# Performance work log

Measured on AMD Instinct MI355X. Metric: run time of the kernel, lower is better.

Reference implementation:

```python
import jax, jax.numpy as jnp
import numpy as np

B, L, S, H, E, D = 4, 2048, 2048, 8, 64, 64

def setup_inputs() -> dict:
    key = jax.random.key(0)
    kq, kk, kv = jax.random.split(key, 3)
    queries = jax.random.normal(kq, (B, L, H, E), dtype=jnp.float32)
    keys = jax.random.normal(kk, (B, S, H, E), dtype=jnp.float32)
    values = jax.random.normal(kv, (B, S, H, D), dtype=jnp.float32)
    # TriangularCausalMask: True above the diagonal (positions to mask)
    causal = jnp.triu(jnp.ones((L, S), dtype=bool), k=1)
    attn_mask = jnp.broadcast_to(causal[None, None], (B, 1, L, S))
    return {"queries": queries, "keys": keys, "values": values, "attn_mask": attn_mask}

def reference(queries, keys, values, attn_mask):
    scale = 1.0 / jnp.sqrt(jnp.asarray(E, queries.dtype))
    # scores: [B,H,L,S]
    scores = jnp.einsum('blhe,bshe->bhls', queries, keys)
    neg_inf = jnp.asarray(-jnp.inf, scores.dtype)
    scores = jnp.where(attn_mask, neg_inf, scores)
    A = jax.nn.softmax(scale * scores, axis=-1)
    # dropout is identity in eval mode
    V = jnp.einsum('bhls,bshd->blhd', A, values)
    return V
```

## Files before the change

kernel.cpp:

```cpp
#include <hip/hip_runtime.h>
#include <math.h>

typedef __attribute__((ext_vector_type(8))) short bf16x8;
typedef __attribute__((ext_vector_type(4))) float f32x4;
typedef __attribute__((ext_vector_type(4))) unsigned int u32x4;

#define B_ 4
#define L_ 2048
#define S_ 2048
#define H_ 8
#define E_ 64
#define D_ 64
#define NT_ 32
#define TILE_BYTES 16384
#define WS_NEEDED ((size_t)B_ * H_ * NT_ * TILE_BYTES)
#define SCL (0.125f * 1.44269504088896f)

__device__ __forceinline__ unsigned short f2bf(float x) {
    unsigned int u = __builtin_bit_cast(unsigned int, x);
    u += 0x7fffu + ((u >> 16) & 1u);
    return (unsigned short)(u >> 16);
}
__device__ __forceinline__ int rho(int r) {
    return (r & 32) | (((r >> 2) & 1) << 4) | (((r >> 3) & 3) << 2) | (r & 3);
}

__global__ __launch_bounds__(256) void prep_kv(const float* __restrict__ K,
                                               const float* __restrict__ V,
                                               unsigned short* __restrict__ ws)
{
    __shared__ __align__(16) unsigned short vt[64][80];
    const int tid = threadIdx.x;
    const int bid = blockIdx.x;
    const int kt  = bid >> 5;
    const int bh  = (((bid >> 3) & 3) << 3) | (bid & 7);
    const int b   = bh >> 3, h = bh & 7;
    const int s0  = kt * 64;
    const int r   = tid >> 2;
    const int e0  = (tid & 3) * 16;

    const float* krow = K + (((size_t)(b * S_ + s0 + r)) * H_ + h) * E_ + e0;
    const float* vrow = V + (((size_t)(b * S_ + s0 + r)) * H_ + h) * D_ + e0;
    char* tile = (char*)(ws) + ((size_t)(bh * NT_ + kt) * TILE_BYTES);

    unsigned short kb[16];
    #pragma unroll
    for (int i = 0; i < 4; ++i) {
        f32x4 k4 = *(const f32x4*)(krow + i * 4);
        #pragma unroll
        for (int jq = 0; jq < 4; ++jq) kb[i * 4 + jq] = f2bf(k4[jq]);
    }
    {
        const int rr = rho(r);
        const int m  = (rr & 7) << 4;
        char* kbase = tile + rr * 128;
        u32x4 lo, hi;
        #pragma unroll
        for (int jq = 0; jq < 4; ++jq) {
            lo[jq] = (unsigned)kb[2 * jq] | ((unsigned)kb[2 * jq + 1] << 16);
            hi[jq] = (unsigned)kb[8 + 2 * jq] | ((unsigned)kb[9 + 2 * jq] << 16);
        }
        *(u32x4*)(kbase + ((2 * e0) ^ m))      = lo;
        *(u32x4*)(kbase + ((2 * e0 + 16) ^ m)) = hi;
    }
    #pragma unroll
    for (int i = 0; i < 4; ++i) {
        f32x4 v4 = *(const f32x4*)(vrow + i * 4);
        #pragma unroll
        for (int jq = 0; jq < 4; ++jq) vt[e0 + i * 4 + jq][r] = f2bf(v4[jq]);
    }
    __syncthreads();
    {
        const int d  = tid >> 2;
        const int c0 = (tid & 3) * 16;
        const int m  = (d & 7) << 4;
        char* vbase = tile + 8192 + d * 128;
        u32x4 lo = *(const u32x4*)&vt[d][c0];
        u32x4 hi = *(const u32x4*)&vt[d][c0 + 8];
        *(u32x4*)(vbase + ((2 * c0) ^ m))      = lo;
        *(u32x4*)(vbase + ((2 * c0 + 16) ^ m)) = hi;
    }
}

#define GL16(dst, p, o) asm volatile("global_load_dwordx4 %0, %1, off offset:" o \
                                     : "=&v"(dst) : "v"(p) : "memory")

#define ISSUE_K() do { \
    GL16(ka[0], pKa, "-3072"); GL16(ka[1], pKb, "-3072"); \
    GL16(ka[2], pKa, "-1024"); GL16(ka[3], pKb, "-1024"); \
    GL16(ka[4], pKa, "1024");  GL16(ka[5], pKb, "1024");  \
    GL16(ka[6], pKa, "3072");  GL16(ka[7], pKb, "3072"); } while (0)

#define ISSUE_V() do { \
    GL16(vb[0], pVa, "-3072"); GL16(vb[1], pVb, "-3072"); \
    GL16(vb[2], pVa, "-1024"); GL16(vb[3], pVb, "-1024"); \
    GL16(vb[4], pVa, "1024");  GL16(vb[5], pVb, "1024");  \
    GL16(vb[6], pVa, "3072");  GL16(vb[7], pVb, "3072"); } while (0)

__device__ __forceinline__ void do_tile(
    const float* __restrict__ Q, const char* __restrict__ tb,
    int b0, int h, int qt, int nt, int lq, int g, float* __restrict__ O)
{
    int qrow[2];
    qrow[0] = qt * 32 + lq;
    qrow[1] = qt * 32 + 16 + lq;

    bf16x8 qf[2][2];
    #pragma unroll
    for (int qs = 0; qs < 2; ++qs) {
        const float* qptr = Q + (((size_t)(b0 * L_ + qrow[qs])) * H_ + h) * E_;
        #pragma unroll
        for (int eb = 0; eb < 2; ++eb) {
            const float* pq = qptr + eb * 32 + g * 8;
            f32x4 a = *(const f32x4*)pq;
            f32x4 b = *(const f32x4*)(pq + 4);
            bf16x8 qv;
            #pragma unroll
            for (int k = 0; k < 4; ++k) {
                qv[k]     = (short)f2bf(a[k] * SCL);
                qv[4 + k] = (short)f2bf(b[k] * SCL);
            }
            qf[qs][eb] = qv;
        }
    }

    const int mm  = (lq & 7) << 4;
    const char* pKa = tb + lq * 128 + ((16 * g) ^ mm) + 3072;
    const char* pKb = tb + lq * 128 + ((64 + 16 * g) ^ mm) + 3072;
    const char* pVa = pKa + 8192;
    const char* pVb = pKb + 8192;

    u32x4 ka[8], vb[8];
    f32x4 acc[2][4] = {};
    float ls[2] = {0.f, 0.f};

    ISSUE_K();
    ISSUE_V();

    for (int kt = 0; kt < nt; ++kt) {
        asm volatile("s_waitcnt vmcnt(8)" ::: "memory");
        __builtin_amdgcn_sched_barrier(0);

        f32x4 sc[2][4];
        __builtin_amdgcn_s_setprio(1);
        #pragma unroll
        for (int st = 0; st < 4; ++st) {
            bf16x8 k0 = __builtin_bit_cast(bf16x8, ka[2 * st]);
            bf16x8 k1 = __builtin_bit_cast(bf16x8, ka[2 * st + 1]);
            #pragma unroll
            for (int qs = 0; qs < 2; ++qs) {
                f32x4 z = {0.f, 0.f, 0.f, 0.f};
                f32x4 cc = __builtin_amdgcn_mfma_f32_16x16x32_bf16(k0, qf[qs][0], z, 0, 0, 0);
                sc[qs][st] = __builtin_amdgcn_mfma_f32_16x16x32_bf16(k1, qf[qs][1], cc, 0, 0, 0);
            }
        }
        __builtin_amdgcn_s_setprio(0);

        const bool hasnext = (kt + 1 < nt);
        if (hasnext) { pKa += TILE_BYTES; pKb += TILE_BYTES; ISSUE_K(); }

        const int kv0 = kt * 64;
        u32x4 pw[2][2];
        #pragma unroll
        for (int qs = 0; qs < 2; ++qs) {
            #pragma unroll
            for (int st = 0; st < 4; ++st) {
                f32x4 cc = sc[qs][st];
                if (kt == nt - 1) {
                    #pragma unroll
                    for (int r = 0; r < 4; ++r) {
                        const int kv = kv0 + 32 * (st >> 1) + 8 * g + 4 * (st & 1) + r;
                        if (kv > qrow[qs]) cc[r] = -INFINITY;
                    }
                }
                f32x4 ev;
                #pragma unroll
                for (int r = 0; r < 4; ++r)
                    asm("v_exp_f32 %0, %1" : "=v"(ev[r]) : "v"(cc[r]));
                ls[qs] += (ev[0] + ev[1]) + (ev[2] + ev[3]);
                asm("v_cvt_pk_bf16_f32 %0, %1, %2" : "=v"(pw[qs][st >> 1][2 * (st & 1)])     : "v"(ev[0]), "v"(ev[1]));
                asm("v_cvt_pk_bf16_f32 %0, %1, %2" : "=v"(pw[qs][st >> 1][2 * (st & 1) + 1]) : "v"(ev[2]), "v"(ev[3]));
            }
        }

        if (hasnext) asm volatile("s_waitcnt vmcnt(8)" ::: "memory");
        else         asm volatile("s_waitcnt vmcnt(0)" ::: "memory");
        __builtin_amdgcn_sched_barrier(0);

        __builtin_amdgcn_s_setprio(1);
        #pragma unroll
        for (int dt = 0; dt < 4; ++dt) {
            bf16x8 v0 = __builtin_bit_cast(bf16x8, vb[2 * dt]);
            bf16x8 v1 = __builtin_bit_cast(bf16x8, vb[2 * dt + 1]);
            #pragma unroll
            for (int qs = 0; qs < 2; ++qs) {
                acc[qs][dt] = __builtin_amdgcn_mfma_f32_16x16x32_bf16(v0, __builtin_bit_cast(bf16x8, pw[qs][0]), acc[qs][dt], 0, 0, 0);
                acc[qs][dt] = __builtin_amdgcn_mfma_f32_16x16x32_bf16(v1, __builtin_bit_cast(bf16x8, pw[qs][1]), acc[qs][dt], 0, 0, 0);
            }
        }
        __builtin_amdgcn_s_setprio(0);

        if (hasnext) { pVa += TILE_BYTES; pVb += TILE_BYTES; ISSUE_V(); }
    }

    #pragma unroll
    for (int qs = 0; qs < 2; ++qs) {
        float l = ls[qs] + __shfl_xor(ls[qs], 16);
        l += __shfl_xor(l, 32);
        const float inv = 1.0f / l;
        float* op = O + (((size_t)(b0 * L_ + qrow[qs])) * H_ + h) * D_;
        #pragma unroll
        for (int dt = 0; dt < 4; ++dt) {
            f32x4 o;
            #pragma unroll
            for (int r = 0; r < 4; ++r) o[r] = acc[qs][dt][r] * inv;
            *(f32x4*)(op + dt * 16 + 4 * g) = o;
        }
    }
}

__global__ __launch_bounds__(128, 2) void attn8(const float* __restrict__ Q,
                                                const unsigned short* __restrict__ ws,
                                                float* __restrict__ O)
{
    const int tid  = threadIdx.x;
    const int lane = tid & 63;
    const int w    = tid >> 6;
    const int lq   = lane & 15;
    const int g    = lane >> 4;

    const int bid = blockIdx.x;
    const int bh  = bid & 31;
    const int jj  = bid >> 5;
    const int b0  = bh >> 3, h = bh & 7;

    const int p   = jj * 2 + w;
    const int ntA = (p >> 1) + 1;
    const int ntB = ((63 - p) >> 1) + 1;

    const char* tb = (const char*)ws + (size_t)bh * NT_ * TILE_BYTES;

    do_tile(Q, tb, b0, h, p,      ntA, lq, g, O);
    do_tile(Q, tb, b0, h, 63 - p, ntB, lq, g, O);
}

#define KPITCH 72
__global__ __launch_bounds__(256, 2) void attn_fwd_fb(
    const float* __restrict__ Q, const float* __restrict__ K,
    const float* __restrict__ V, float* __restrict__ O)
{
    __shared__ unsigned short Klds[64 * KPITCH];
    __shared__ unsigned short Vlds[64 * KPITCH];
    const int tid = threadIdx.x, lane = tid & 63, w = tid >> 6;
    const int lq = lane & 15, g = lane >> 4;
    const int bid = blockIdx.x, qb = bid & 31, bh = bid >> 5;
    const int b0 = bh >> 3, h = bh & 7;
    const int q0 = qb * 64, qrow = q0 + w * 16 + lq;
    const float* qptr = Q + ((size_t)(b0 * L_ + qrow) * H_ + h) * E_;
    bf16x8 qf[2];
    #pragma unroll
    for (int eb = 0; eb < 2; ++eb) {
        const float* pp = qptr + eb * 32 + g * 8;
        f32x4 a = *(const f32x4*)pp; f32x4 b = *(const f32x4*)(pp + 4);
        bf16x8 q;
        #pragma unroll
        for (int jq = 0; jq < 4; ++jq) { q[jq] = (short)f2bf(a[jq] * 0.125f); q[4 + jq] = (short)f2bf(b[jq] * 0.125f); }
        qf[eb] = q;
    }
    const int tr = tid >> 2, tc = tid & 3;
    const int rh = rho(tr);
    f32x4 acc[4] = {};
    float mrow = -INFINITY, lrow = 0.f;
    for (int kt = 0; kt < qb + 1; ++kt) {
        const int kv0 = kt * 64;
        __syncthreads();
        {
            const float* krow = K + ((size_t)((b0 * S_ + kv0 + tr)) * H_ + h) * E_;
            const float* vrow = V + ((size_t)((b0 * S_ + kv0 + tr)) * H_ + h) * D_;
            #pragma unroll
            for (int i = 0; i < 4; ++i) {
                const int e0 = tc * 4 + i * 16;
                f32x4 k4 = *(const f32x4*)(krow + e0);
                unsigned int lo = (unsigned)f2bf(k4[0]) | ((unsigned)f2bf(k4[1]) << 16);
                unsigned int hi = (unsigned)f2bf(k4[2]) | ((unsigned)f2bf(k4[3]) << 16);
                *(uint2*)&Klds[rh * KPITCH + e0] = make_uint2(lo, hi);
                f32x4 v4 = *(const f32x4*)(vrow + e0);
                #pragma unroll
                for (int k2 = 0; k2 < 4; ++k2) Vlds[(e0 + k2) * KPITCH + tr] = f2bf(v4[k2]);
            }
        }
        __syncthreads();
        f32x4 sc[4];
        #pragma unroll
        for (int st = 0; st < 4; ++st) {
            const unsigned short* kr = &Klds[(st * 16 + lq) * KPITCH];
            bf16x8 ka0 = *(const bf16x8*)(kr + 8 * g);
            bf16x8 ka1 = *(const bf16x8*)(kr + 32 + 8 * g);
            f32x4 cc = {0.f, 0.f, 0.f, 0.f};
            cc = __builtin_amdgcn_mfma_f32_16x16x32_bf16(ka0, qf[0], cc, 0, 0, 0);
            cc = __builtin_amdgcn_mfma_f32_16x16x32_bf16(ka1, qf[1], cc, 0, 0, 0);
            sc[st] = cc;
        }
        float tmax = -INFINITY;
        #pragma unroll
        for (int st = 0; st < 4; ++st) {
            const int kvb = kv0 + 32 * (st >> 1) + 8 * g + 4 * (st & 1);
            #pragma unroll
            for (int r = 0; r < 4; ++r) { if (kvb + r > qrow) sc[st][r] = -INFINITY; tmax = fmaxf(tmax, sc[st][r]); }
        }
        tmax = fmaxf(tmax, __shfl_xor(tmax, 16));
        tmax = fmaxf(tmax, __shfl_xor(tmax, 32));
        const float mnew = fmaxf(mrow, tmax);
        const float corr = __expf(mrow - mnew);
        float pv[4][4]; float tsum = 0.f;
        #pragma unroll
        for (int st = 0; st < 4; ++st)
            #pragma unroll
            for (int r = 0; r < 4; ++r) { float e = __expf(sc[st][r] - mnew); pv[st][r] = e; tsum += e; }
        tsum += __shfl_xor(tsum, 16); tsum += __shfl_xor(tsum, 32);
        lrow = lrow * corr + tsum; mrow = mnew;
        #pragma unroll
        for (int dt = 0; dt < 4; ++dt)
            #pragma unroll
            for (int r = 0; r < 4; ++r) acc[dt][r] *= corr;
        bf16x8 pb[2];
        #pragma unroll
        for (int bb = 0; bb < 2; ++bb)
            #pragma unroll
            for (int s = 0; s < 2; ++s)
                #pragma unroll
                for (int r = 0; r < 4; ++r) pb[bb][4 * s + r] = (short)f2bf(pv[2 * bb + s][r]);
        #pragma unroll
        for (int bb = 0; bb < 2; ++bb)
            #pragma unroll
            for (int dt = 0; dt < 4; ++dt) {
                bf16x8 va = *(const bf16x8*)&Vlds[(dt * 16 + lq) * KPITCH + 32 * bb + 8 * g];
                acc[dt] = __builtin_amdgcn_mfma_f32_16x16x32_bf16(va, pb[bb], acc[dt], 0, 0, 0);
            }
    }
    const float inv = 1.0f / lrow;
    float* optr = O + ((size_t)(b0 * L_ + qrow) * H_ + h) * D_;
    #pragma unroll
    for (int dt = 0; dt < 4; ++dt) {
        f32x4 o;
        #pragma unroll
        for (int r = 0; r < 4; ++r) o[r] = acc[dt][r] * inv;
        *(f32x4*)(optr + dt * 16 + 4 * g) = o;
    }
}

extern "C" void kernel_launch(void* const* d_in, const int* in_sizes, int n_in,
                              void* d_out, int out_size, void* d_ws, size_t ws_size,
                              hipStream_t stream) {
    const float* Q = (const float*)d_in[0];
    const float* K = (const float*)d_in[1];
    const float* V = (const float*)d_in[2];
    float* O = (float*)d_out;
    if (ws_size >= WS_NEEDED) {
        prep_kv<<<dim3(B_ * H_ * NT_), 256, 0, stream>>>(K, V, (unsigned short*)d_ws);
        attn8<<<dim3(512), 128, 0, stream>>>(Q, (const unsigned short*)d_ws, O);
    } else {
        attn_fwd_fb<<<dim3(B_ * H_ * 32), 256, 0, stream>>>(Q, K, V, O);
    }
}
```

Baseline: 49.08 us.

## Share K/V tiles across 8 waves via LDS double buffering with global_load_lds

```diff
diff --git a/kernel.cpp b/kernel.cpp
--- a/kernel.cpp
+++ b/kernel.cpp
@@ -23,6 +23,10 @@
 }
 __device__ __forceinline__ int rho(int r) {
     return (r & 32) | (((r >> 2) & 1) << 4) | (((r >> 3) & 3) << 2) | (r & 3);
+}
+__device__ __forceinline__ void gload16(const void* g, void* l) {
+    __builtin_amdgcn_global_load_lds((const __attribute__((address_space(1))) unsigned int*)g,
+                                     (__attribute__((address_space(3))) unsigned int*)l, 16, 0, 0);
 }
 
 __global__ __launch_bounds__(256) void prep_kv(const float* __restrict__ K,
@@ -82,28 +86,29 @@
     }
 }
 
-#define GL16(dst, p, o) asm volatile("global_load_dwordx4 %0, %1, off offset:" o \
-                                     : "=&v"(dst) : "v"(p) : "memory")
-
-#define ISSUE_K() do { \
-    GL16(ka[0], pKa, "-3072"); GL16(ka[1], pKb, "-3072"); \
-    GL16(ka[2], pKa, "-1024"); GL16(ka[3], pKb, "-1024"); \
-    GL16(ka[4], pKa, "1024");  GL16(ka[5], pKb, "1024");  \
-    GL16(ka[6], pKa, "3072");  GL16(ka[7], pKb, "3072"); } while (0)
-
-#define ISSUE_V() do { \
-    GL16(vb[0], pVa, "-3072"); GL16(vb[1], pVb, "-3072"); \
-    GL16(vb[2], pVa, "-1024"); GL16(vb[3], pVb, "-1024"); \
-    GL16(vb[4], pVa, "1024");  GL16(vb[5], pVb, "1024");  \
-    GL16(vb[6], pVa, "3072");  GL16(vb[7], pVb, "3072"); } while (0)
-
-__device__ __forceinline__ void do_tile(
-    const float* __restrict__ Q, const char* __restrict__ tb,
-    int b0, int h, int qt, int nt, int lq, int g, float* __restrict__ O)
+__global__ __launch_bounds__(512, 4) void attn9(const float* __restrict__ Q,
+                                                const unsigned short* __restrict__ ws,
+                                                float* __restrict__ O)
 {
+    __shared__ __align__(16) char lds[2][TILE_BYTES];
+
+    const int tid  = threadIdx.x;
+    const int lane = tid & 63;
+    const int w    = tid >> 6;
+    const int lq   = lane & 15;
+    const int g    = lane >> 4;
+
+    const int bid = blockIdx.x;
+    const int bh  = bid & 31;
+    const int j   = bid >> 5;
+    const int b0  = bh >> 3, h = bh & 7;
+
+    const int q0  = j * 256 + w * 32;
+    const int nt  = 4 * j + 4;
+    const int dkt = 4 * j + (w >> 1);
     int qrow[2];
-    qrow[0] = qt * 32 + lq;
-    qrow[1] = qt * 32 + 16 + lq;
+    qrow[0] = q0 + lq;
+    qrow[1] = q0 + 16 + lq;
 
     bf16x8 qf[2][2];
     #pragma unroll
@@ -124,83 +129,83 @@
         }
     }
 
-    const int mm  = (lq & 7) << 4;
-    const char* pKa = tb + lq * 128 + ((16 * g) ^ mm) + 3072;
-    const char* pKb = tb + lq * 128 + ((64 + 16 * g) ^ mm) + 3072;
-    const char* pVa = pKa + 8192;
-    const char* pVb = pKb + 8192;
-
-    u32x4 ka[8], vb[8];
     f32x4 acc[2][4] = {};
     float ls[2] = {0.f, 0.f};
 
-    ISSUE_K();
-    ISSUE_V();
-
+    const char* tb = (const char*)ws + (size_t)bh * NT_ * TILE_BYTES;
+
+    gload16(tb + tid * 16, &lds[0][tid * 16]);
+    gload16(tb + 8192 + tid * 16, &lds[0][8192 + tid * 16]);
+
+    int cur = 0;
     for (int kt = 0; kt < nt; ++kt) {
-        asm volatile("s_waitcnt vmcnt(8)" ::: "memory");
+        if (kt + 1 < nt) {
+            const char* gp = tb + (size_t)(kt + 1) * TILE_BYTES;
+            char* lp = &lds[cur ^ 1][0];
+            gload16(gp + tid * 16, lp + tid * 16);
+            gload16(gp + 8192 + tid * 16, lp + 8192 + tid * 16);
+            asm volatile("s_waitcnt vmcnt(2)" ::: "memory");
+        } else {
+            asm volatile("s_waitcnt vmcnt(0)" ::: "memory");
+        }
+        __builtin_amdgcn_s_barrier();
         __builtin_amdgcn_sched_barrier(0);
 
-        f32x4 sc[2][4];
-        __builtin_amdgcn_s_setprio(1);
-        #pragma unroll
-        for (int st = 0; st < 4; ++st) {
-            bf16x8 k0 = __builtin_bit_cast(bf16x8, ka[2 * st]);
-            bf16x8 k1 = __builtin_bit_cast(bf16x8, ka[2 * st + 1]);
-            #pragma unroll
-            for (int qs = 0; qs < 2; ++qs) {
-                f32x4 z = {0.f, 0.f, 0.f, 0.f};
-                f32x4 cc = __builtin_amdgcn_mfma_f32_16x16x32_bf16(k0, qf[qs][0], z, 0, 0, 0);
-                sc[qs][st] = __builtin_amdgcn_mfma_f32_16x16x32_bf16(k1, qf[qs][1], cc, 0, 0, 0);
-            }
-        }
-        __builtin_amdgcn_s_setprio(0);
-
-        const bool hasnext = (kt + 1 < nt);
-        if (hasnext) { pKa += TILE_BYTES; pKb += TILE_BYTES; ISSUE_K(); }
-
-        const int kv0 = kt * 64;
-        u32x4 pw[2][2];
-        #pragma unroll
-        for (int qs = 0; qs < 2; ++qs) {
+        if (kt <= dkt) {
+            const char* Kl = &lds[cur][0];
+            const char* Vl = &lds[cur][8192];
+            const int kv0 = kt * 64;
+
+            u32x4 pw[2][2];
             #pragma unroll
             for (int st = 0; st < 4; ++st) {
-                f32x4 cc = sc[qs][st];
-                if (kt == nt - 1) {
+                const int row = st * 16 + lq;
+                const int mm = (row & 7) << 4;
+                const char* kr = Kl + row * 128;
+                bf16x8 k0 = *(const bf16x8*)(kr + ((16 * g) ^ mm));
+                bf16x8 k1 = *(const bf16x8*)(kr + ((64 + 16 * g) ^ mm));
+                #pragma unroll
+                for (int qs = 0; qs < 2; ++qs) {
+                    f32x4 z = {0.f, 0.f, 0.f, 0.f};
+                    __builtin_amdgcn_s_setprio(1);
+                    f32x4 cc = __builtin_amdgcn_mfma_f32_16x16x32_bf16(k0, qf[qs][0], z, 0, 0, 0);
+                    cc = __builtin_amdgcn_mfma_f32_16x16x32_bf16(k1, qf[qs][1], cc, 0, 0, 0);
+                    __builtin_amdgcn_s_setprio(0);
+                    if (kt == dkt) {
+                        #pragma unroll
+                        for (int r = 0; r < 4; ++r) {
+                            const int kv = kv0 + 32 * (st >> 1) + 8 * g + 4 * (st & 1) + r;
+                            if (kv > qrow[qs]) cc[r] = -INFINITY;
+                        }
+                    }
+                    f32x4 ev;
                     #pragma unroll
-                    for (int r = 0; r < 4; ++r) {
-                        const int kv = kv0 + 32 * (st >> 1) + 8 * g + 4 * (st & 1) + r;
-                        if (kv > qrow[qs]) cc[r] = -INFINITY;
-                    }
+                    for (int r = 0; r < 4; ++r)
+                        asm("v_exp_f32 %0, %1" : "=v"(ev[r]) : "v"(cc[r]));
+                    ls[qs] += (ev[0] + ev[1]) + (ev[2] + ev[3]);
+                    asm("v_cvt_pk_bf16_f32 %0, %1, %2" : "=v"(pw[qs][st >> 1][2 * (st & 1)])     : "v"(ev[0]), "v"(ev[1]));
+                    asm("v_cvt_pk_bf16_f32 %0, %1, %2" : "=v"(pw[qs][st >> 1][2 * (st & 1) + 1]) : "v"(ev[2]), "v"(ev[3]));
                 }
-                f32x4 ev;
+            }
+
+            #pragma unroll
+            for (int dt = 0; dt < 4; ++dt) {
+                const int row = dt * 16 + lq;
+                const int mm = (row & 7) << 4;
+                bf16x8 v0 = *(const bf16x8*)(Vl + row * 128 + ((16 * g) ^ mm));
+                bf16x8 v1 = *(const bf16x8*)(Vl + row * 128 + ((64 + 16 * g) ^ mm));
+                __builtin_amdgcn_s_setprio(1);
                 #pragma unroll
-                for (int r = 0; r < 4; ++r)
-                    asm("v_exp_f32 %0, %1" : "=v"(ev[r]) : "v"(cc[r]));
-                ls[qs] += (ev[0] + ev[1]) + (ev[2] + ev[3]);
-                asm("v_cvt_pk_bf16_f32 %0, %1, %2" : "=v"(pw[qs][st >> 1][2 * (st & 1)])     : "v"(ev[0]), "v"(ev[1]));
-                asm("v_cvt_pk_bf16_f32 %0, %1, %2" : "=v"(pw[qs][st >> 1][2 * (st & 1) + 1]) : "v"(ev[2]), "v"(ev[3]));
-            }
-        }
-
-        if (hasnext) asm volatile("s_waitcnt vmcnt(8)" ::: "memory");
-        else         asm volatile("s_waitcnt vmcnt(0)" ::: "memory");
-        __builtin_amdgcn_sched_barrier(0);
-
-        __builtin_amdgcn_s_setprio(1);
-        #pragma unroll
-        for (int dt = 0; dt < 4; ++dt) {
-            bf16x8 v0 = __builtin_bit_cast(bf16x8, vb[2 * dt]);
-            bf16x8 v1 = __builtin_bit_cast(bf16x8, vb[2 * dt + 1]);
-            #pragma unroll
-            for (int qs = 0; qs < 2; ++qs) {
-                acc[qs][dt] = __builtin_amdgcn_mfma_f32_16x16x32_bf16(v0, __builtin_bit_cast(bf16x8, pw[qs][0]), acc[qs][dt], 0, 0, 0);
-                acc[qs][dt] = __builtin_amdgcn_mfma_f32_16x16x32_bf16(v1, __builtin_bit_cast(bf16x8, pw[qs][1]), acc[qs][dt], 0, 0, 0);
-            }
-        }
-        __builtin_amdgcn_s_setprio(0);
-
-        if (hasnext) { pVa += TILE_BYTES; pVb += TILE_BYTES; ISSUE_V(); }
+                for (int qs = 0; qs < 2; ++qs) {
+                    acc[qs][dt] = __builtin_amdgcn_mfma_f32_16x16x32_bf16(v0, __builtin_bit_cast(bf16x8, pw[qs][0]), acc[qs][dt], 0, 0, 0);
+                    acc[qs][dt] = __builtin_amdgcn_mfma_f32_16x16x32_bf16(v1, __builtin_bit_cast(bf16x8, pw[qs][1]), acc[qs][dt], 0, 0, 0);
+                }
+                __builtin_amdgcn_s_setprio(0);
+            }
+        }
+
+        __builtin_amdgcn_s_barrier();
+        cur ^= 1;
     }
 
     #pragma unroll
@@ -217,31 +222,6 @@
             *(f32x4*)(op + dt * 16 + 4 * g) = o;
         }
     }
-}
-
-__global__ __launch_bounds__(128, 2) void attn8(const float* __restrict__ Q,
-                                                const unsigned short* __restrict__ ws,
-                                                float* __restrict__ O)
-{
-    const int tid  = threadIdx.x;
-    const int lane = tid & 63;
-    const int w    = tid >> 6;
-    const int lq   = lane & 15;
-    const int g    = lane >> 4;
-
-    const int bid = blockIdx.x;
-    const int bh  = bid & 31;
-    const int jj  = bid >> 5;
-    const int b0  = bh >> 3, h = bh & 7;
-
-    const int p   = jj * 2 + w;
-    const int ntA = (p >> 1) + 1;
-    const int ntB = ((63 - p) >> 1) + 1;
-
-    const char* tb = (const char*)ws + (size_t)bh * NT_ * TILE_BYTES;
-
-    do_tile(Q, tb, b0, h, p,      ntA, lq, g, O);
-    do_tile(Q, tb, b0, h, 63 - p, ntB, lq, g, O);
 }
 
 #define KPITCH 72
@@ -358,7 +338,7 @@
     float* O = (float*)d_out;
     if (ws_size >= WS_NEEDED) {
         prep_kv<<<dim3(B_ * H_ * NT_), 256, 0, stream>>>(K, V, (unsigned short*)d_ws);
-        attn8<<<dim3(512), 128, 0, stream>>>(Q, (const unsigned short*)d_ws, O);
+        attn9<<<dim3(256), 512, 0, stream>>>(Q, (const unsigned short*)d_ws, O);
     } else {
         attn_fwd_fb<<<dim3(B_ * H_ * 32), 256, 0, stream>>>(Q, K, V, O);
     }
```

Result: slower. 56.20 us (+14.5%).

## Double-buffer K/V register prefetch two tiles ahead and use 4-wave blocks

Applied to the files above, without the earlier changes.

```diff
diff --git a/kernel.cpp b/kernel.cpp
--- a/kernel.cpp
+++ b/kernel.cpp
@@ -85,22 +85,89 @@
 #define GL16(dst, p, o) asm volatile("global_load_dwordx4 %0, %1, off offset:" o \
                                      : "=&v"(dst) : "v"(p) : "memory")
 
-#define ISSUE_K() do { \
-    GL16(ka[0], pKa, "-3072"); GL16(ka[1], pKb, "-3072"); \
-    GL16(ka[2], pKa, "-1024"); GL16(ka[3], pKb, "-1024"); \
-    GL16(ka[4], pKa, "1024");  GL16(ka[5], pKb, "1024");  \
-    GL16(ka[6], pKa, "3072");  GL16(ka[7], pKb, "3072"); } while (0)
-
-#define ISSUE_V() do { \
-    GL16(vb[0], pVa, "-3072"); GL16(vb[1], pVb, "-3072"); \
-    GL16(vb[2], pVa, "-1024"); GL16(vb[3], pVb, "-1024"); \
-    GL16(vb[4], pVa, "1024");  GL16(vb[5], pVb, "1024");  \
-    GL16(vb[6], pVa, "3072");  GL16(vb[7], pVb, "3072"); } while (0)
-
-__device__ __forceinline__ void do_tile(
+#define ISSUE8(ARR, BA, BB) do { \
+    GL16(ARR[0], BA, "-3072"); GL16(ARR[1], BB, "-3072"); \
+    GL16(ARR[2], BA, "-1024"); GL16(ARR[3], BB, "-1024"); \
+    GL16(ARR[4], BA, "1024");  GL16(ARR[5], BB, "1024");  \
+    GL16(ARR[6], BA, "3072");  GL16(ARR[7], BB, "3072"); } while (0)
+
+#define TRIP_HALF(KARR, VARR, KT) do { \
+    asm volatile("s_waitcnt vmcnt(24)" ::: "memory"); \
+    __builtin_amdgcn_sched_barrier(0); \
+    const bool act_ = (KT) < nt; \
+    f32x4 sc[2][4]; \
+    if (act_) { \
+        __builtin_amdgcn_s_setprio(1); \
+        _Pragma("unroll") \
+        for (int st = 0; st < 4; ++st) { \
+            bf16x8 k0 = __builtin_bit_cast(bf16x8, KARR[2 * st]); \
+            bf16x8 k1 = __builtin_bit_cast(bf16x8, KARR[2 * st + 1]); \
+            _Pragma("unroll") \
+            for (int qs = 0; qs < 2; ++qs) { \
+                f32x4 z = {0.f, 0.f, 0.f, 0.f}; \
+                f32x4 cc = __builtin_amdgcn_mfma_f32_16x16x32_bf16(k0, qf[qs][0], z, 0, 0, 0); \
+                sc[qs][st] = __builtin_amdgcn_mfma_f32_16x16x32_bf16(k1, qf[qs][1], cc, 0, 0, 0); \
+            } \
+        } \
+        __builtin_amdgcn_s_setprio(0); \
+    } \
+    { int ti = (KT) + 2; if (ti > nm1) ti = nm1; \
+      const char* ba_ = tb + (size_t)ti * TILE_BYTES + o_a; \
+      const char* bb_ = tb + (size_t)ti * TILE_BYTES + o_b; \
+      ISSUE8(KARR, ba_, bb_); } \
+    u32x4 pw[2][2]; \
+    if (act_) { \
+        const int kv0 = (KT) * 64; \
+        const bool maskit = ((KT) == nm1); \
+        _Pragma("unroll") \
+        for (int qs = 0; qs < 2; ++qs) { \
+            _Pragma("unroll") \
+            for (int st = 0; st < 4; ++st) { \
+                f32x4 cc = sc[qs][st]; \
+                if (maskit) { \
+                    _Pragma("unroll") \
+                    for (int r = 0; r < 4; ++r) { \
+                        const int kv = kv0 + 32 * (st >> 1) + 8 * g + 4 * (st & 1) + r; \
+                        if (kv > qrow[qs]) cc[r] = -INFINITY; \
+                    } \
+                } \
+                f32x4 ev; \
+                _Pragma("unroll") \
+                for (int r = 0; r < 4; ++r) \
+                    asm("v_exp_f32 %0, %1" : "=v"(ev[r]) : "v"(cc[r])); \
+                ls[qs] += (ev[0] + ev[1]) + (ev[2] + ev[3]); \
+                asm("v_cvt_pk_bf16_f32 %0, %1, %2" : "=v"(pw[qs][st >> 1][2 * (st & 1)])     : "v"(ev[0]), "v"(ev[1])); \
+                asm("v_cvt_pk_bf16_f32 %0, %1, %2" : "=v"(pw[qs][st >> 1][2 * (st & 1) + 1]) : "v"(ev[2]), "v"(ev[3])); \
+            } \
+        } \
+    } \
+    asm volatile("s_waitcnt vmcnt(24)" ::: "memory"); \
+    __builtin_amdgcn_sched_barrier(0); \
+    if (act_) { \
+        __builtin_amdgcn_s_setprio(1); \
+        _Pragma("unroll") \
+        for (int dt = 0; dt < 4; ++dt) { \
+            bf16x8 v0 = __builtin_bit_cast(bf16x8, VARR[2 * dt]); \
+            bf16x8 v1 = __builtin_bit_cast(bf16x8, VARR[2 * dt + 1]); \
+            _Pragma("unroll") \
+            for (int qs = 0; qs < 2; ++qs) { \
+                acc[qs][dt] = __builtin_amdgcn_mfma_f32_16x16x32_bf16(v0, __builtin_bit_cast(bf16x8, pw[qs][0]), acc[qs][dt], 0, 0, 0); \
+                acc[qs][dt] = __builtin_amdgcn_mfma_f32_16x16x32_bf16(v1, __builtin_bit_cast(bf16x8, pw[qs][1]), acc[qs][dt], 0, 0, 0); \
+            } \
+        } \
+        __builtin_amdgcn_s_setprio(0); \
+    } \
+    { int ti = (KT) + 2; if (ti > nm1) ti = nm1; \
+      const char* ba_ = tb + (size_t)ti * TILE_BYTES + 8192 + o_a; \
+      const char* bb_ = tb + (size_t)ti * TILE_BYTES + 8192 + o_b; \
+      ISSUE8(VARR, ba_, bb_); } \
+} while (0)
+
+__device__ __forceinline__ void do_tile16(
     const float* __restrict__ Q, const char* __restrict__ tb,
     int b0, int h, int qt, int nt, int lq, int g, float* __restrict__ O)
 {
+    const int nm1 = nt - 1;
     int qrow[2];
     qrow[0] = qt * 32 + lq;
     qrow[1] = qt * 32 + 16 + lq;
@@ -125,83 +192,31 @@
     }
 
     const int mm  = (lq & 7) << 4;
-    const char* pKa = tb + lq * 128 + ((16 * g) ^ mm) + 3072;
-    const char* pKb = tb + lq * 128 + ((64 + 16 * g) ^ mm) + 3072;
-    const char* pVa = pKa + 8192;
-    const char* pVb = pKb + 8192;
-
-    u32x4 ka[8], vb[8];
+    const int o_a = lq * 128 + ((16 * g) ^ mm) + 3072;
+    const int o_b = lq * 128 + ((64 + 16 * g) ^ mm) + 3072;
+
+    u32x4 kA[8], kB[8], vA[8], vB[8];
     f32x4 acc[2][4] = {};
     float ls[2] = {0.f, 0.f};
 
-    ISSUE_K();
-    ISSUE_V();
-
-    for (int kt = 0; kt < nt; ++kt) {
-        asm volatile("s_waitcnt vmcnt(8)" ::: "memory");
-        __builtin_amdgcn_sched_barrier(0);
-
-        f32x4 sc[2][4];
-        __builtin_amdgcn_s_setprio(1);
-        #pragma unroll
-        for (int st = 0; st < 4; ++st) {
-            bf16x8 k0 = __builtin_bit_cast(bf16x8, ka[2 * st]);
-            bf16x8 k1 = __builtin_bit_cast(bf16x8, ka[2 * st + 1]);
-            #pragma unroll
-            for (int qs = 0; qs < 2; ++qs) {
-                f32x4 z = {0.f, 0.f, 0.f, 0.f};
-                f32x4 cc = __builtin_amdgcn_mfma_f32_16x16x32_bf16(k0, qf[qs][0], z, 0, 0, 0);
-                sc[qs][st] = __builtin_amdgcn_mfma_f32_16x16x32_bf16(k1, qf[qs][1], cc, 0, 0, 0);
-            }
-        }
-        __builtin_amdgcn_s_setprio(0);
-
-        const bool hasnext = (kt + 1 < nt);
-        if (hasnext) { pKa += TILE_BYTES; pKb += TILE_BYTES; ISSUE_K(); }
-
-        const int kv0 = kt * 64;
-        u32x4 pw[2][2];
-        #pragma unroll
-        for (int qs = 0; qs < 2; ++qs) {
-            #pragma unroll
-            for (int st = 0; st < 4; ++st) {
-                f32x4 cc = sc[qs][st];
-                if (kt == nt - 1) {
-                    #pragma unroll
-                    for (int r = 0; r < 4; ++r) {
-                        const int kv = kv0 + 32 * (st >> 1) + 8 * g + 4 * (st & 1) + r;
-                        if (kv > qrow[qs]) cc[r] = -INFINITY;
-                    }
-                }
-                f32x4 ev;
-                #pragma unroll
-                for (int r = 0; r < 4; ++r)
-                    asm("v_exp_f32 %0, %1" : "=v"(ev[r]) : "v"(cc[r]));
-                ls[qs] += (ev[0] + ev[1]) + (ev[2] + ev[3]);
-                asm("v_cvt_pk_bf16_f32 %0, %1, %2" : "=v"(pw[qs][st >> 1][2 * (st & 1)])     : "v"(ev[0]), "v"(ev[1]));
-                asm("v_cvt_pk_bf16_f32 %0, %1, %2" : "=v"(pw[qs][st >> 1][2 * (st & 1) + 1]) : "v"(ev[2]), "v"(ev[3]));
-            }
-        }
-
-        if (hasnext) asm volatile("s_waitcnt vmcnt(8)" ::: "memory");
-        else         asm volatile("s_waitcnt vmcnt(0)" ::: "memory");
-        __builtin_amdgcn_sched_barrier(0);
-
-        __builtin_amdgcn_s_setprio(1);
-        #pragma unroll
-        for (int dt = 0; dt < 4; ++dt) {
-            bf16x8 v0 = __builtin_bit_cast(bf16x8, vb[2 * dt]);
-            bf16x8 v1 = __builtin_bit_cast(bf16x8, vb[2 * dt + 1]);
-            #pragma unroll
-            for (int qs = 0; qs < 2; ++qs) {
-                acc[qs][dt] = __builtin_amdgcn_mfma_f32_16x16x32_bf16(v0, __builtin_bit_cast(bf16x8, pw[qs][0]), acc[qs][dt], 0, 0, 0);
-                acc[qs][dt] = __builtin_amdgcn_mfma_f32_16x16x32_bf16(v1, __builtin_bit_cast(bf16x8, pw[qs][1]), acc[qs][dt], 0, 0, 0);
-            }
-        }
-        __builtin_amdgcn_s_setprio(0);
-
-        if (hasnext) { pVa += TILE_BYTES; pVb += TILE_BYTES; ISSUE_V(); }
-    }
+    {
+        const char* a0 = tb + o_a;
+        const char* b0_ = tb + o_b;
+        ISSUE8(kA, a0, b0_);
+        ISSUE8(vA, a0 + 8192, b0_ + 8192);
+        int t1 = (1 > nm1) ? nm1 : 1;
+        const char* a1 = tb + (size_t)t1 * TILE_BYTES + o_a;
+        const char* b1 = tb + (size_t)t1 * TILE_BYTES + o_b;
+        ISSUE8(kB, a1, b1);
+        ISSUE8(vB, a1 + 8192, b1 + 8192);
+    }
+
+    for (int kt = 0; kt < nt; kt += 2) {
+        TRIP_HALF(kA, vA, kt);
+        TRIP_HALF(kB, vB, kt + 1);
+    }
+    asm volatile("s_waitcnt vmcnt(0)" ::: "memory");
+    __builtin_amdgcn_sched_barrier(0);
 
     #pragma unroll
     for (int qs = 0; qs < 2; ++qs) {
@@ -219,9 +234,9 @@
     }
 }
 
-__global__ __launch_bounds__(128, 2) void attn8(const float* __restrict__ Q,
-                                                const unsigned short* __restrict__ ws,
-                                                float* __restrict__ O)
+__global__ __launch_bounds__(256, 1) void attn16(const float* __restrict__ Q,
+                                                 const unsigned short* __restrict__ ws,
+                                                 float* __restrict__ O)
 {
     const int tid  = threadIdx.x;
     const int lane = tid & 63;
@@ -231,17 +246,17 @@
 
     const int bid = blockIdx.x;
     const int bh  = bid & 31;
-    const int jj  = bid >> 5;
+    const int j   = bid >> 5;
     const int b0  = bh >> 3, h = bh & 7;
 
-    const int p   = jj * 2 + w;
+    const int p   = j * 4 + w;
     const int ntA = (p >> 1) + 1;
     const int ntB = ((63 - p) >> 1) + 1;
 
     const char* tb = (const char*)ws + (size_t)bh * NT_ * TILE_BYTES;
 
-    do_tile(Q, tb, b0, h, p,      ntA, lq, g, O);
-    do_tile(Q, tb, b0, h, 63 - p, ntB, lq, g, O);
+    do_tile16(Q, tb, b0, h, p,      ntA, lq, g, O);
+    do_tile16(Q, tb, b0, h, 63 - p, ntB, lq, g, O);
 }
 
 #define KPITCH 72
@@ -262,10 +277,10 @@
     for (int eb = 0; eb < 2; ++eb) {
         const float* pp = qptr + eb * 32 + g * 8;
         f32x4 a = *(const f32x4*)pp; f32x4 b = *(const f32x4*)(pp + 4);
-        bf16x8 q;
-        #pragma unroll
-        for (int jq = 0; jq < 4; ++jq) { q[jq] = (short)f2bf(a[jq] * 0.125f); q[4 + jq] = (short)f2bf(b[jq] * 0.125f); }
-        qf[eb] = q;
+        bf16x8 qv;
+        #pragma unroll
+        for (int jq = 0; jq < 4; ++jq) { qv[jq] = (short)f2bf(a[jq] * 0.125f); qv[4 + jq] = (short)f2bf(b[jq] * 0.125f); }
+        qf[eb] = qv;
     }
     const int tr = tid >> 2, tc = tid & 3;
     const int rh = rho(tr);
@@ -358,7 +373,7 @@
     float* O = (float*)d_out;
     if (ws_size >= WS_NEEDED) {
         prep_kv<<<dim3(B_ * H_ * NT_), 256, 0, stream>>>(K, V, (unsigned short*)d_ws);
-        attn8<<<dim3(512), 128, 0, stream>>>(Q, (const unsigned short*)d_ws, O);
+        attn16<<<dim3(256), 256, 0, stream>>>(Q, (const unsigned short*)d_ws, O);
     } else {
         attn_fwd_fb<<<dim3(B_ * H_ * 32), 256, 0, stream>>>(Q, K, V, O);
     }
```

Measured after the change: 52.40 us. +6.8%, slower.
